# Kernel tuning notes

Hardware: AMD Instinct MI355X
Metric: run time of the kernel (lower is better)

The kernel has to match this reference:

```python
import jax, jax.numpy as jnp
import numpy as np

EMBED = 256
HEADS = 8
LEVELS = 4
POINTS = 4
HEAD_DIM = EMBED // HEADS
SHAPES = [(100, 100), (50, 50), (25, 25), (13, 13)]  # (H, W) per level
NUM_KEYS = sum(h * w for h, w in SHAPES)  # 13294
LEVEL_STARTS = np.cumsum([0] + [h * w for h, w in SHAPES])[:-1]
B, Q = 8, 900


def _offset_bias():
    # Faithful reproduction of the torch _reset_parameters sampling_offsets bias.
    th = np.arange(HEADS, dtype=np.float32) * (2.0 * np.pi / HEADS)
    g = np.stack([np.cos(th), np.sin(th)], -1)
    g = g / np.abs(g).max(-1, keepdims=True)
    g = np.tile(g[:, None, None, :], (1, LEVELS, POINTS, 1))
    g = g * np.arange(1, POINTS + 1, dtype=np.float32)[None, None, :, None]
    return jnp.asarray(g.reshape(-1), dtype=jnp.float32)


def setup_inputs() -> dict:
    key = jax.random.key(0)
    ks = jax.random.split(key, 12)
    s = 1.0 / np.sqrt(EMBED)
    return {
        "query": jax.random.normal(ks[0], (B, Q, EMBED), jnp.float32),
        "reference_points": jax.random.uniform(ks[1], (B, Q, LEVELS, 2), jnp.float32),
        "value": jax.random.normal(ks[2], (B, NUM_KEYS, EMBED), jnp.float32),
        "spatial_shapes": jnp.asarray(np.array(SHAPES, dtype=np.int32)),
        "level_start_index": jnp.asarray(LEVEL_STARTS.astype(np.int32)),
        "W_off": jax.random.normal(ks[3], (EMBED, HEADS * LEVELS * POINTS * 2), jnp.float32) * 0.01,
        "b_off": _offset_bias(),
        "W_attn": jax.random.normal(ks[4], (EMBED, HEADS * LEVELS * POINTS), jnp.float32) * 0.01,
        "b_attn": jnp.zeros((HEADS * LEVELS * POINTS,), jnp.float32),
        "W_val": jax.random.normal(ks[5], (EMBED, EMBED), jnp.float32) * s,
        "b_val": jnp.zeros((EMBED,), jnp.float32),
        "W_out": jax.random.normal(ks[6], (EMBED, EMBED), jnp.float32) * s,
        "b_out": jnp.zeros((EMBED,), jnp.float32),
    }


def _bilinear(vflat, x, y, H, W):
    # vflat: [BH, H*W, D]; x, y: [BH, Q, P] in unnormalized pixel coords.
    # grid_sample(mode='bilinear', padding_mode='zeros', align_corners=False)
    BH, Qn, Pn = x.shape
    D = vflat.shape[-1]
    x0f = jnp.floor(x); y0f = jnp.floor(y)
    wx = x - x0f; wy = y - y0f
    x0 = x0f.astype(jnp.int32); y0 = y0f.astype(jnp.int32)

    def gather(xi, yi):
        inb = (xi >= 0) & (xi < W) & (yi >= 0) & (yi < H)
        idx = jnp.clip(yi, 0, H - 1) * W + jnp.clip(xi, 0, W - 1)
        g = jnp.take_along_axis(vflat, idx.reshape(BH, Qn * Pn, 1), axis=1)
        return g.reshape(BH, Qn, Pn, D) * inb[..., None].astype(vflat.dtype)

    v00 = gather(x0, y0)
    v01 = gather(x0 + 1, y0)
    v10 = gather(x0, y0 + 1)
    v11 = gather(x0 + 1, y0 + 1)
    return (v00 * ((1 - wx) * (1 - wy))[..., None]
            + v01 * (wx * (1 - wy))[..., None]
            + v10 * ((1 - wx) * wy)[..., None]
            + v11 * (wx * wy)[..., None])


def _msda(value_hd, shapes_np, starts_np, loc, attw):
    # value_hd: [B, K, H, D]; loc: [B, Q, H, L, P, 2]; attw: [B, Q, H, L, P]
    Bn, K, Hn, D = value_hd.shape
    Qn, Pn = loc.shape[1], loc.shape[4]
    out = jnp.zeros((Bn * Hn, Qn, D), value_hd.dtype)
    for l, (Hl, Wl) in enumerate(shapes_np):
        s = int(starts_np[l])
        v = value_hd[:, s:s + Hl * Wl]                      # [B, Hl*Wl, H, D]
        v = v.reshape(Bn, Hl * Wl, Hn, D).transpose(0, 2, 1, 3)
        vflat = v.reshape(Bn * Hn, Hl * Wl, D)
        # sampling_grid = 2*loc - 1; grid_sample align_corners=False -> x = loc*W - 0.5
        lx = loc[:, :, :, l, :, 0].transpose(0, 2, 1, 3).reshape(Bn * Hn, Qn, Pn)
        ly = loc[:, :, :, l, :, 1].transpose(0, 2, 1, 3).reshape(Bn * Hn, Qn, Pn)
        samp = _bilinear(vflat, lx * Wl - 0.5, ly * Hl - 0.5, Hl, Wl)  # [BH,Q,P,D]
        w = attw[:, :, :, l, :].transpose(0, 2, 1, 3).reshape(Bn * Hn, Qn, Pn)
        out = out + jnp.einsum('bqpd,bqp->bqd', samp, w)
    return out.reshape(Bn, Hn, Qn, D).transpose(0, 2, 1, 3).reshape(Bn, Qn, Hn * D)


def reference(query, reference_points, value, spatial_shapes, level_start_index,
              W_off, b_off, W_attn, b_attn, W_val, b_val, W_out, b_out):
    shapes_np = np.asarray(spatial_shapes)
    starts_np = np.asarray(level_start_index)
    Bn, Qn, _ = query.shape
    K = value.shape[1]

    v = value @ W_val + b_val                              # [B, K, E]
    v = v.reshape(Bn, K, HEADS, HEAD_DIM)

    off = (query @ W_off + b_off).reshape(Bn, Qn, HEADS, LEVELS, POINTS, 2)
    aw = (query @ W_attn + b_attn).reshape(Bn, Qn, HEADS, LEVELS * POINTS)
    aw = jax.nn.softmax(aw, axis=-1).reshape(Bn, Qn, HEADS, LEVELS, POINTS)

    # offset_normalizer = (W, H) per level
    norm = jnp.asarray(shapes_np[:, ::-1].astype(np.float32)).reshape(1, 1, 1, LEVELS, 1, 2)
    loc = reference_points[:, :, None, :, None, :] + off / norm  # [B,Q,H,L,P,2]

    out = _msda(v, shapes_np, starts_np, loc, aw)          # [B, Q, E]
    return out @ W_out + b_out
```

## Files before the change

### kernel.cpp

```cpp
#include <hip/hip_runtime.h>
#include <hip/hip_bf16.h>
#include <math.h>
#include <type_traits>

#define BATCH 8
#define QLEN 900
#define HEADS 8
#define LEVELS 4
#define POINTS 4
#define NUM_KEYS 13294
#define BQ (BATCH * QLEN)
#define MROWS_V (BATCH * NUM_KEYS)

__constant__ const int c_LH[4] = {100, 50, 25, 13};
__constant__ const int c_LW[4] = {100, 50, 25, 13};
__constant__ const int c_LS[4] = {0, 10000, 12500, 13125};

typedef __attribute__((ext_vector_type(8))) short bfrag;
typedef __attribute__((ext_vector_type(4))) float ffrag;

static __device__ __forceinline__ unsigned short f2bf(float f) {
    __hip_bfloat16 h = __float2bfloat16(f);
    return *(unsigned short*)&h;
}
static __device__ __forceinline__ float bf2f(unsigned int u16) {
    unsigned int v = u16 << 16;
    float f;
    __builtin_memcpy(&f, &v, 4);
    return f;
}

__global__ __launch_bounds__(256)
void prep_kernel(const float* __restrict__ W_val, const float* __restrict__ W_off,
                 const float* __restrict__ W_attn, const float* __restrict__ W_out,
                 const float* __restrict__ b_off, const float* __restrict__ b_attn,
                 unsigned short* __restrict__ Wv, unsigned short* __restrict__ Woa,
                 unsigned short* __restrict__ Wo, float* __restrict__ boa) {
    const int id = blockIdx.x * 256 + threadIdx.x;
    if (id < 65536) {
        const int n = id >> 8, k = id & 255;
        Wv[id] = f2bf(W_val[k * 256 + n]);
    } else if (id < 131072) {
        const int t = id - 65536;
        const int n = t >> 8, k = t & 255;
        Woa[t] = f2bf(W_off[k * 256 + n]);
    } else if (id < 163840) {
        const int t = id - 131072;
        const int n = t >> 8, k = t & 255;
        Woa[65536 + t] = f2bf(W_attn[k * 128 + n]);
    } else if (id < 229376) {
        const int t = id - 163840;
        const int n = t >> 8, k = t & 255;
        Wo[t] = f2bf(W_out[k * 256 + n]);
    } else if (id < 229760) {
        const int t = id - 229376;
        boa[t] = (t < 256) ? b_off[t] : b_attn[t - 256];
    }
}

#define VS_GRID 512

__global__ __launch_bounds__(256, 2)
void gemm_val_stream(const float* __restrict__ A, const unsigned short* __restrict__ WT,
                     const float* __restrict__ bias, unsigned short* __restrict__ C,
                     int M) {
    const int tid = threadIdx.x;
    const int wave = tid >> 6;
    const int lane = tid & 63;
    const int ln = lane & 15;
    const int quad = lane >> 4;
    const int n0 = wave * 64;

    bfrag b[4][8];
#pragma unroll
    for (int j = 0; j < 4; ++j) {
        const unsigned short* bp = WT + (size_t)(n0 + j * 16 + ln) * 256 + quad * 8;
#pragma unroll
        for (int ks = 0; ks < 8; ++ks)
            b[j][ks] = *(const bfrag*)(bp + ks * 32);
    }

    const int ntiles = M >> 4;
    int tile = blockIdx.x;
    if (tile >= ntiles) return;

    float4 f[8][2];
    {
        const float* ap = A + (size_t)(tile * 16 + ln) * 256 + quad * 8;
#pragma unroll
        for (int ks = 0; ks < 8; ++ks) {
            f[ks][0] = *(const float4*)(ap + ks * 32);
            f[ks][1] = *(const float4*)(ap + ks * 32 + 4);
        }
    }

    while (tile < ntiles) {
        bfrag a[8];
#pragma unroll
        for (int ks = 0; ks < 8; ++ks) {
            const float v[8] = {f[ks][0].x, f[ks][0].y, f[ks][0].z, f[ks][0].w,
                                f[ks][1].x, f[ks][1].y, f[ks][1].z, f[ks][1].w};
#pragma unroll
            for (int i = 0; i < 8; ++i) a[ks][i] = (short)f2bf(v[i]);
        }

        const int next = tile + VS_GRID;
        const int pn = (next < ntiles) ? next : tile;
        {
            const float* ap = A + (size_t)(pn * 16 + ln) * 256 + quad * 8;
#pragma unroll
            for (int ks = 0; ks < 8; ++ks) {
                f[ks][0] = *(const float4*)(ap + ks * 32);
                f[ks][1] = *(const float4*)(ap + ks * 32 + 4);
            }
        }

        ffrag acc[4];
#pragma unroll
        for (int j = 0; j < 4; ++j) acc[j] = (ffrag){0.f, 0.f, 0.f, 0.f};
#pragma unroll
        for (int ks = 0; ks < 8; ++ks) {
#pragma unroll
            for (int j = 0; j < 4; ++j)
                acc[j] = __builtin_amdgcn_mfma_f32_16x16x32_bf16(a[ks], b[j][ks], acc[j], 0, 0, 0);
        }

        const int rb = tile * 16;
#pragma unroll
        for (int j = 0; j < 4; ++j) {
            const int col = n0 + j * 16 + ln;
            const float bb = bias[col];
#pragma unroll
            for (int r = 0; r < 4; ++r) {
                C[(size_t)(rb + quad * 4 + r) * 256 + col] = f2bf(acc[j][r] + bb);
            }
        }
        tile = next;
    }
}

#define GST 72

template <typename AT, typename CT>
__global__ __launch_bounds__(256)
void gemm_mfma(const AT* __restrict__ A, const unsigned short* __restrict__ WT,
               const float* __restrict__ bias, CT* __restrict__ C,
               int M, int ldc) {
    __shared__ unsigned short As[64 * GST];
    __shared__ unsigned short Bs[128 * GST];
    const int tid = threadIdx.x;
    const int wave = tid >> 6;
    const int lane = tid & 63;
    const int ln = lane & 15;
    const int quad = lane >> 4;
    const int m0 = blockIdx.x * 64;
    const int n0 = blockIdx.y * 128;

    ffrag acc[8];
#pragma unroll
    for (int j = 0; j < 8; ++j) acc[j] = (ffrag){0.f, 0.f, 0.f, 0.f};

    const int ar = tid >> 2;
    const int akc = (tid & 3) * 16;
    const int brow = tid >> 1;
    const int bkc = (tid & 1) * 32;
    const bool a_ok = (m0 + ar) < M;
    const AT* a_src = A + (size_t)(m0 + ar) * 256 + akc;
    const unsigned short* b_src = WT + (size_t)(n0 + brow) * 256 + bkc;

    for (int k0 = 0; k0 < 256; k0 += 64) {
        unsigned short* adst = &As[ar * GST + akc];
        if constexpr (std::is_same<AT, float>::value) {
            float4 f0, f1, f2, f3;
            if (a_ok) {
                const float4* p = (const float4*)(a_src + k0);
                f0 = p[0]; f1 = p[1]; f2 = p[2]; f3 = p[3];
            } else {
                f0 = make_float4(0.f, 0.f, 0.f, 0.f);
                f1 = f0; f2 = f0; f3 = f0;
            }
            float v[16] = {f0.x, f0.y, f0.z, f0.w, f1.x, f1.y, f1.z, f1.w,
                           f2.x, f2.y, f2.z, f2.w, f3.x, f3.y, f3.z, f3.w};
            unsigned short u[16];
#pragma unroll
            for (int i = 0; i < 16; ++i) u[i] = f2bf(v[i]);
            ((uint4*)adst)[0] = ((uint4*)u)[0];
            ((uint4*)adst)[1] = ((uint4*)u)[1];
        } else {
            uint4 u0, u1;
            if (a_ok) {
                const uint4* p = (const uint4*)(a_src + k0);
                u0 = p[0]; u1 = p[1];
            } else {
                u0 = make_uint4(0, 0, 0, 0);
                u1 = u0;
            }
            ((uint4*)adst)[0] = u0;
            ((uint4*)adst)[1] = u1;
        }
        {
            const uint4* src = (const uint4*)(b_src + k0);
            uint4* dst = (uint4*)&Bs[brow * GST + bkc];
#pragma unroll
            for (int i = 0; i < 4; ++i) dst[i] = src[i];
        }
        __syncthreads();

#pragma unroll
        for (int ks = 0; ks < 2; ++ks) {
            const int koff = ks * 32 + quad * 8;
            bfrag af = *(const bfrag*)&As[(wave * 16 + ln) * GST + koff];
#pragma unroll
            for (int j = 0; j < 8; ++j) {
                bfrag bf = *(const bfrag*)&Bs[(j * 16 + ln) * GST + koff];
                acc[j] = __builtin_amdgcn_mfma_f32_16x16x32_bf16(af, bf, acc[j], 0, 0, 0);
            }
        }
        __syncthreads();
    }

#pragma unroll
    for (int j = 0; j < 8; ++j) {
        const int col = n0 + j * 16 + ln;
        const float bb = bias[col];
#pragma unroll
        for (int r = 0; r < 4; ++r) {
            const int row = m0 + wave * 16 + quad * 4 + r;
            if (row < M) {
                const float v = acc[j][r] + bb;
                if constexpr (std::is_same<CT, unsigned short>::value) {
                    C[(size_t)row * ldc + col] = f2bf(v);
                } else {
                    C[(size_t)row * ldc + col] = v;
                }
            }
        }
    }
}

__global__ __launch_bounds__(256, 4)
void msda_sample_kernel(const float* __restrict__ offattn,
                        const float* __restrict__ rp,
                        const unsigned short* __restrict__ vb,
                        unsigned short* __restrict__ outb) {
    const int bq0 = blockIdx.x * 8;
    const int tid = threadIdx.x;

    __shared__ float s_w[8][128];
    __shared__ float s_x[8][128];
    __shared__ float s_y[8][128];

#pragma unroll
    for (int i = 0; i < 4; ++i) {
        const int e = i * 256 + tid;
        const int q = e >> 7, t = e & 127;
        s_w[q][t] = offattn[(size_t)(bq0 + q) * 384 + 256 + t];
    }
    __syncthreads();

    if (tid < 64) {
        const int q = tid >> 3, h = tid & 7;
        float m = -1e30f;
#pragma unroll
        for (int i = 0; i < 16; ++i) m = fmaxf(m, s_w[q][h * 16 + i]);
        float e[16];
        float s = 0.f;
#pragma unroll
        for (int i = 0; i < 16; ++i) {
            e[i] = expf(s_w[q][h * 16 + i] - m);
            s += e[i];
        }
        const float inv = 1.f / s;
#pragma unroll
        for (int i = 0; i < 16; ++i) s_w[q][h * 16 + i] = e[i] * inv;
    }

#pragma unroll
    for (int i = 0; i < 4; ++i) {
        const int e = i * 256 + tid;
        const int q = e >> 7, t = e & 127;
        const int h = t >> 4, l = (t >> 2) & 3, p = t & 3;
        const int bq = bq0 + q;
        const float2 off = *(const float2*)(offattn + (size_t)bq * 384 + h * 32 + l * 8 + p * 2);
        const float Wl = (float)c_LW[l];
        const float Hl = (float)c_LH[l];
        const float rx = rp[((size_t)bq * 4 + l) * 2 + 0];
        const float ry = rp[((size_t)bq * 4 + l) * 2 + 1];
        s_x[q][t] = (rx + off.x / Wl) * Wl - 0.5f;
        s_y[q][t] = (ry + off.y / Hl) * Hl - 0.5f;
    }
    __syncthreads();

    const int q = tid >> 5;
    const int s = tid & 31;
    const int h = s >> 2;
    const int dp = s & 3;
    const int bq = bq0 + q;
    const int b = bq / QLEN;
    const unsigned short* vbase = vb + (size_t)b * NUM_KEYS * 256 + h * 32 + dp * 8;

    float acc[8];
#pragma unroll
    for (int d = 0; d < 8; ++d) acc[d] = 0.f;

#pragma unroll
    for (int l = 0; l < LEVELS; ++l) {
        const int Hl = c_LH[l];
        const int Wl = c_LW[l];
        const int s0 = c_LS[l];
#pragma unroll 2
        for (int p = 0; p < POINTS; ++p) {
            const int t2 = h * 16 + l * 4 + p;
            const float x = s_x[q][t2];
            const float y = s_y[q][t2];
            const float w = s_w[q][t2];
            const float x0f = floorf(x);
            const float y0f = floorf(y);
            const float wx = x - x0f;
            const float wy = y - y0f;
            const int x0 = (int)x0f;
            const int y0 = (int)y0f;
            const float mx0 = ((unsigned)x0 < (unsigned)Wl) ? 1.f : 0.f;
            const float mx1 = ((unsigned)(x0 + 1) < (unsigned)Wl) ? 1.f : 0.f;
            const float my0 = ((unsigned)y0 < (unsigned)Hl) ? 1.f : 0.f;
            const float my1 = ((unsigned)(y0 + 1) < (unsigned)Hl) ? 1.f : 0.f;
            const int xc0 = min(max(x0, 0), Wl - 1);
            const int xc1 = min(max(x0 + 1, 0), Wl - 1);
            const int yc0 = min(max(y0, 0), Hl - 1);
            const int yc1 = min(max(y0 + 1, 0), Hl - 1);
            const float a00 = w * (1.f - wx) * (1.f - wy) * mx0 * my0;
            const float a01 = w * wx * (1.f - wy) * mx1 * my0;
            const float a10 = w * (1.f - wx) * wy * mx0 * my1;
            const float a11 = w * wx * wy * mx1 * my1;
            const size_t k00 = (size_t)(s0 + yc0 * Wl + xc0) * 256;
            const size_t k01 = (size_t)(s0 + yc0 * Wl + xc1) * 256;
            const size_t k10 = (size_t)(s0 + yc1 * Wl + xc0) * 256;
            const size_t k11 = (size_t)(s0 + yc1 * Wl + xc1) * 256;
            const uint4 r00 = *(const uint4*)(vbase + k00);
            const uint4 r01 = *(const uint4*)(vbase + k01);
            const uint4 r10 = *(const uint4*)(vbase + k10);
            const uint4 r11 = *(const uint4*)(vbase + k11);
            const unsigned int w00[4] = {r00.x, r00.y, r00.z, r00.w};
            const unsigned int w01[4] = {r01.x, r01.y, r01.z, r01.w};
            const unsigned int w10[4] = {r10.x, r10.y, r10.z, r10.w};
            const unsigned int w11[4] = {r11.x, r11.y, r11.z, r11.w};
#pragma unroll
            for (int i = 0; i < 4; ++i) {
                const float v00l = bf2f(w00[i] & 0xffffu), v00h = bf2f(w00[i] >> 16);
                const float v01l = bf2f(w01[i] & 0xffffu), v01h = bf2f(w01[i] >> 16);
                const float v10l = bf2f(w10[i] & 0xffffu), v10h = bf2f(w10[i] >> 16);
                const float v11l = bf2f(w11[i] & 0xffffu), v11h = bf2f(w11[i] >> 16);
                acc[i * 2 + 0] = fmaf(a00, v00l, fmaf(a01, v01l, fmaf(a10, v10l, fmaf(a11, v11l, acc[i * 2 + 0]))));
                acc[i * 2 + 1] = fmaf(a00, v00h, fmaf(a01, v01h, fmaf(a10, v10h, fmaf(a11, v11h, acc[i * 2 + 1]))));
            }
        }
    }

    unsigned short o[8];
#pragma unroll
    for (int d = 0; d < 8; ++d) o[d] = f2bf(acc[d]);
    *(uint4*)(outb + (size_t)bq * 256 + h * 32 + dp * 8) = *(uint4*)o;
}

extern "C" void kernel_launch(void* const* d_in, const int* in_sizes, int n_in,
                              void* d_out, int out_size, void* d_ws, size_t ws_size,
                              hipStream_t stream) {
    const float* query  = (const float*)d_in[0];
    const float* rp     = (const float*)d_in[1];
    const float* value  = (const float*)d_in[2];
    const float* W_off  = (const float*)d_in[5];
    const float* b_off  = (const float*)d_in[6];
    const float* W_attn = (const float*)d_in[7];
    const float* b_attn = (const float*)d_in[8];
    const float* W_val  = (const float*)d_in[9];
    const float* b_val  = (const float*)d_in[10];
    const float* W_out  = (const float*)d_in[11];
    const float* b_out  = (const float*)d_in[12];
    float* out = (float*)d_out;

    char* w = (char*)d_ws;
    unsigned short* ws_vb = (unsigned short*)w;
    w += (size_t)MROWS_V * 256 * 2;
    float* ws_offattn = (float*)w;
    w += (size_t)BQ * 384 * 4;
    unsigned short* ws_msda = (unsigned short*)w;
    w += (size_t)BQ * 256 * 2;
    unsigned short* ws_Wv = (unsigned short*)w;  w += 256 * 256 * 2;
    unsigned short* ws_Woa = (unsigned short*)w; w += 384 * 256 * 2;
    unsigned short* ws_Wo = (unsigned short*)w;  w += 256 * 256 * 2;
    float* ws_boa = (float*)w;

    prep_kernel<<<898, 256, 0, stream>>>(W_val, W_off, W_attn, W_out,
                                         b_off, b_attn, ws_Wv, ws_Woa, ws_Wo, ws_boa);

    gemm_val_stream<<<VS_GRID, 256, 0, stream>>>(value, ws_Wv, b_val, ws_vb, MROWS_V);

    {
        dim3 grid((BQ + 63) / 64, 3);
        gemm_mfma<float, float><<<grid, 256, 0, stream>>>(
            query, ws_Woa, ws_boa, ws_offattn, BQ, 384);
    }
    msda_sample_kernel<<<BQ / 8, 256, 0, stream>>>(ws_offattn, rp, ws_vb, ws_msda);

    {
        dim3 grid((BQ + 63) / 64, 2);
        gemm_mfma<unsigned short, float><<<grid, 256, 0, stream>>>(
            ws_msda, ws_Wo, b_out, out, BQ, 256);
    }
}
```

Before: 274.7 us.

## Stage value tiles through swizzled LDS triple buffer with coalesced loads

```diff
diff --git a/kernel.cpp b/kernel.cpp
--- a/kernel.cpp
+++ b/kernel.cpp
@@ -11,6 +11,9 @@
 #define NUM_KEYS 13294
 #define BQ (BATCH * QLEN)
 #define MROWS_V (BATCH * NUM_KEYS)
+#define VTILES (MROWS_V / 16)
+#define VBLOCKS 512
+#define TPB 13
 
 __constant__ const int c_LH[4] = {100, 50, 25, 13};
 __constant__ const int c_LW[4] = {100, 50, 25, 13};
@@ -28,6 +31,12 @@
     float f;
     __builtin_memcpy(&f, &v, 4);
     return f;
+}
+static __device__ __forceinline__ unsigned long long pack4bf(float4 v) {
+    return (unsigned long long)f2bf(v.x)
+         | ((unsigned long long)f2bf(v.y) << 16)
+         | ((unsigned long long)f2bf(v.z) << 32)
+         | ((unsigned long long)f2bf(v.w) << 48);
 }
 
 __global__ __launch_bounds__(256)
@@ -58,12 +67,10 @@
     }
 }
 
-#define VS_GRID 512
-
 __global__ __launch_bounds__(256, 2)
 void gemm_val_stream(const float* __restrict__ A, const unsigned short* __restrict__ WT,
-                     const float* __restrict__ bias, unsigned short* __restrict__ C,
-                     int M) {
+                     const float* __restrict__ bias, unsigned short* __restrict__ C) {
+    __shared__ __align__(16) unsigned short Abuf[3][16 * 256];
     const int tid = threadIdx.x;
     const int wave = tid >> 6;
     const int lane = tid & 63;
@@ -76,66 +83,84 @@
     for (int j = 0; j < 4; ++j) {
         const unsigned short* bp = WT + (size_t)(n0 + j * 16 + ln) * 256 + quad * 8;
 #pragma unroll
-        for (int ks = 0; ks < 8; ++ks)
-            b[j][ks] = *(const bfrag*)(bp + ks * 32);
-    }
-
-    const int ntiles = M >> 4;
-    int tile = blockIdx.x;
-    if (tile >= ntiles) return;
-
-    float4 f[8][2];
+        for (int ks = 0; ks < 8; ++ks) b[j][ks] = *(const bfrag*)(bp + ks * 32);
+    }
+    float bj[4];
+#pragma unroll
+    for (int j = 0; j < 4; ++j) bj[j] = bias[n0 + j * 16 + ln];
+
+    const int t0 = blockIdx.x * TPB;
+    const int t1 = min(t0 + TPB, VTILES);
+    if (t0 >= t1) return;
+
+    int dsoff[4];
+#pragma unroll
+    for (int i = 0; i < 4; ++i) {
+        const int f = i * 256 + tid;
+        const int r = f >> 6;
+        const int cb = (f & 63) * 8;
+        dsoff[i] = r * 512 + (cb ^ ((r & 7) << 4));
+    }
+
+    const float4* Af4 = (const float4*)A;
+
+    float4 Lp[4];
     {
-        const float* ap = A + (size_t)(tile * 16 + ln) * 256 + quad * 8;
+        const float4* ap = Af4 + (size_t)t0 * 1024 + tid;
+#pragma unroll
+        for (int i = 0; i < 4; ++i) Lp[i] = ap[i * 256];
+    }
+#pragma unroll
+    for (int i = 0; i < 4; ++i)
+        *(unsigned long long*)((char*)&Abuf[0][0] + dsoff[i]) = pack4bf(Lp[i]);
+    if (t0 + 1 < t1) {
+        const float4* ap = Af4 + (size_t)(t0 + 1) * 1024 + tid;
+#pragma unroll
+        for (int i = 0; i < 4; ++i) Lp[i] = ap[i * 256];
+    }
+    asm volatile("s_waitcnt lgkmcnt(0)" ::: "memory");
+    __builtin_amdgcn_s_barrier();
+
+    int rb = 0;
+    for (int t = t0; t < t1; ++t) {
+        const char* abuf = (const char*)&Abuf[rb][0];
+        ffrag acc[4];
+#pragma unroll
+        for (int j = 0; j < 4; ++j) acc[j] = (ffrag){0.f, 0.f, 0.f, 0.f};
 #pragma unroll
         for (int ks = 0; ks < 8; ++ks) {
-            f[ks][0] = *(const float4*)(ap + ks * 32);
-            f[ks][1] = *(const float4*)(ap + ks * 32 + 4);
-        }
-    }
-
-    while (tile < ntiles) {
-        bfrag a[8];
-#pragma unroll
-        for (int ks = 0; ks < 8; ++ks) {
-            const float v[8] = {f[ks][0].x, f[ks][0].y, f[ks][0].z, f[ks][0].w,
-                                f[ks][1].x, f[ks][1].y, f[ks][1].z, f[ks][1].w};
-#pragma unroll
-            for (int i = 0; i < 8; ++i) a[ks][i] = (short)f2bf(v[i]);
-        }
-
-        const int next = tile + VS_GRID;
-        const int pn = (next < ntiles) ? next : tile;
-        {
-            const float* ap = A + (size_t)(pn * 16 + ln) * 256 + quad * 8;
-#pragma unroll
-            for (int ks = 0; ks < 8; ++ks) {
-                f[ks][0] = *(const float4*)(ap + ks * 32);
-                f[ks][1] = *(const float4*)(ap + ks * 32 + 4);
-            }
-        }
-
-        ffrag acc[4];
-#pragma unroll
-        for (int j = 0; j < 4; ++j) acc[j] = (ffrag){0.f, 0.f, 0.f, 0.f};
-#pragma unroll
-        for (int ks = 0; ks < 8; ++ks) {
+            const int ub = (ks * 64 + quad * 16) ^ ((ln & 7) << 4);
+            const bfrag af = *(const bfrag*)(abuf + ln * 512 + ub);
 #pragma unroll
             for (int j = 0; j < 4; ++j)
-                acc[j] = __builtin_amdgcn_mfma_f32_16x16x32_bf16(a[ks], b[j][ks], acc[j], 0, 0, 0);
-        }
-
-        const int rb = tile * 16;
+                acc[j] = __builtin_amdgcn_mfma_f32_16x16x32_bf16(af, b[j][ks], acc[j], 0, 0, 0);
+        }
+
+        if (t + 1 < t1) {
+            const int wb = (rb + 1 == 3) ? 0 : rb + 1;
+            char* dbuf = (char*)&Abuf[wb][0];
+#pragma unroll
+            for (int i = 0; i < 4; ++i)
+                *(unsigned long long*)(dbuf + dsoff[i]) = pack4bf(Lp[i]);
+            if (t + 2 < t1) {
+                const float4* ap = Af4 + (size_t)(t + 2) * 1024 + tid;
+#pragma unroll
+                for (int i = 0; i < 4; ++i) Lp[i] = ap[i * 256];
+            }
+        }
+
+        const int rowb = t * 16 + quad * 4;
 #pragma unroll
         for (int j = 0; j < 4; ++j) {
             const int col = n0 + j * 16 + ln;
-            const float bb = bias[col];
-#pragma unroll
-            for (int r = 0; r < 4; ++r) {
-                C[(size_t)(rb + quad * 4 + r) * 256 + col] = f2bf(acc[j][r] + bb);
-            }
-        }
-        tile = next;
+#pragma unroll
+            for (int r = 0; r < 4; ++r)
+                C[(size_t)(rowb + r) * 256 + col] = f2bf(acc[j][r] + bj[j]);
+        }
+
+        asm volatile("s_waitcnt lgkmcnt(0)" ::: "memory");
+        __builtin_amdgcn_s_barrier();
+        rb = (rb + 1 == 3) ? 0 : rb + 1;
     }
 }
 
@@ -393,7 +418,7 @@
     prep_kernel<<<898, 256, 0, stream>>>(W_val, W_off, W_attn, W_out,
                                          b_off, b_attn, ws_Wv, ws_Woa, ws_Wo, ws_boa);
 
-    gemm_val_stream<<<VS_GRID, 256, 0, stream>>>(value, ws_Wv, b_val, ws_vb, MROWS_V);
+    gemm_val_stream<<<VBLOCKS, 256, 0, stream>>>(value, ws_Wv, b_val, ws_vb);
 
     {
         dim3 grid((BQ + 63) / 64, 3);
```

Measured after the change: 256.0 us. 6.8% less time.
